# Optimization experiments

Measured on AMD Instinct MI355X. Metric: run time of the kernel, lower is better.

Reference implementation:

```python
import jax, jax.numpy as jnp
import numpy as np

ALPHA = 0.154
NUM_CLASSES = 50257
N = 4096

def setup_inputs() -> dict:
    key = jax.random.key(0)
    k1, k2 = jax.random.split(key)
    inputs = jax.random.normal(k1, (N, NUM_CLASSES), dtype=jnp.float32)
    targets = jax.random.randint(k2, (N,), 0, NUM_CLASSES, dtype=jnp.int64 if jax.config.jax_enable_x64 else jnp.int32)
    return {"inputs": inputs, "targets": targets}

def reference(inputs, targets):
    # softmax over classes (last dim), then probability at target class per row
    # log(softmax) computed stably via log_softmax (same math as log(softmax(x)))
    logp = jax.nn.log_softmax(inputs, axis=-1)           # [N, V]
    n = inputs.shape[0]
    logp_t = logp[jnp.arange(n), targets]                # [N], fused gather instead of NxN diag
    scale = 1.0 - ALPHA + ALPHA / float(inputs.shape[-1])
    out = logp_t + jnp.log(jnp.float32(scale))           # log(p_t * scale)
    return -jnp.mean(out)
```

## Files before the change

### kernel.cpp

```cpp
#include <hip/hip_runtime.h>
#include <cstdint>
#include <cstddef>

#define V 50257
#define BLOCK 256
#define UNROLL 8

__device__ __forceinline__ void combine(float& m, float& s, float mo, float so) {
    float m2 = fmaxf(m, mo);
    s = s * __expf(m - m2) + so * __expf(mo - m2);
    m = m2;
}

__device__ __forceinline__ float max4(const float4 v) {
    return fmaxf(fmaxf(v.x, v.y), fmaxf(v.z, v.w));
}

__device__ __forceinline__ float esum4(const float4 v, const float m2) {
    return (__expf(v.x - m2) + __expf(v.y - m2)) + (__expf(v.z - m2) + __expf(v.w - m2));
}

__global__ __launch_bounds__(BLOCK) void sce_row_kernel(
    const float* __restrict__ inputs, const int* __restrict__ targets,
    float* __restrict__ row_out) {
    const int row = blockIdx.x;
    const int tid = threadIdx.x;
    const float* row_ptr = inputs + (size_t)row * V;

    float xt = 0.0f;
    if (tid == 0) xt = row_ptr[targets[row]];

    const int misalign = (int)(((size_t)row * V) & 3);
    const int head = (4 - misalign) & 3;
    const int nvec = (V - head) >> 2;
    const int tail_start = head + (nvec << 2);
    const float4* vp = reinterpret_cast<const float4*>(row_ptr + head);

    float m = -INFINITY, s = 0.0f;

    int i = tid;
    for (; i + (UNROLL - 1) * BLOCK < nvec; i += UNROLL * BLOCK) {
        const float4 a0 = vp[i];
        const float4 a1 = vp[i + 1 * BLOCK];
        const float4 a2 = vp[i + 2 * BLOCK];
        const float4 a3 = vp[i + 3 * BLOCK];
        const float4 a4 = vp[i + 4 * BLOCK];
        const float4 a5 = vp[i + 5 * BLOCK];
        const float4 a6 = vp[i + 6 * BLOCK];
        const float4 a7 = vp[i + 7 * BLOCK];

        const float cm = fmaxf(
            fmaxf(fmaxf(max4(a0), max4(a1)), fmaxf(max4(a2), max4(a3))),
            fmaxf(fmaxf(max4(a4), max4(a5)), fmaxf(max4(a6), max4(a7))));
        const float m2 = fmaxf(m, cm);
        const float r = __expf(m - m2);
        const float e =
            ((esum4(a0, m2) + esum4(a1, m2)) + (esum4(a2, m2) + esum4(a3, m2))) +
            ((esum4(a4, m2) + esum4(a5, m2)) + (esum4(a6, m2) + esum4(a7, m2)));
        s = fmaf(s, r, e);
        m = m2;
    }
    for (; i < nvec; i += BLOCK) {
        const float4 v = vp[i];
        const float mv = max4(v);
        const float m2 = fmaxf(m, mv);
        s = fmaf(s, __expf(m - m2), esum4(v, m2));
        m = m2;
    }
    for (int j = tid; j < head; j += BLOCK) {
        const float v = row_ptr[j];
        const float m2 = fmaxf(m, v);
        s = s * __expf(m - m2) + __expf(v - m2);
        m = m2;
    }
    for (int j = tail_start + tid; j < V; j += BLOCK) {
        const float v = row_ptr[j];
        const float m2 = fmaxf(m, v);
        s = s * __expf(m - m2) + __expf(v - m2);
        m = m2;
    }

    for (int off = 32; off > 0; off >>= 1) {
        const float mo = __shfl_xor(m, off, 64);
        const float so = __shfl_xor(s, off, 64);
        combine(m, s, mo, so);
    }
    __shared__ float sm[BLOCK / 64], ss[BLOCK / 64];
    const int wave = tid >> 6;
    const int lane = tid & 63;
    if (lane == 0) { sm[wave] = m; ss[wave] = s; }
    __syncthreads();
    if (tid == 0) {
        m = sm[0]; s = ss[0];
        #pragma unroll
        for (int w = 1; w < BLOCK / 64; ++w) combine(m, s, sm[w], ss[w]);
        const float log_scale = logf((float)(1.0 - 0.154 + 0.154 / (double)V));
        row_out[row] = (xt - m - logf(s)) + log_scale;
    }
}

__global__ __launch_bounds__(BLOCK) void sce_final_kernel(
    const float* __restrict__ row_vals, float* __restrict__ out, int n) {
    float sum = 0.0f;
    for (int i = threadIdx.x; i < n; i += BLOCK) sum += row_vals[i];
    for (int off = 32; off > 0; off >>= 1) sum += __shfl_xor(sum, off, 64);
    __shared__ float ssum[BLOCK / 64];
    const int wave = threadIdx.x >> 6;
    const int lane = threadIdx.x & 63;
    if (lane == 0) ssum[wave] = sum;
    __syncthreads();
    if (threadIdx.x == 0) {
        float t = 0.0f;
        #pragma unroll
        for (int w = 0; w < BLOCK / 64; ++w) t += ssum[w];
        out[0] = -t / (float)n;
    }
}

extern "C" void kernel_launch(void* const* d_in, const int* in_sizes, int n_in,
                              void* d_out, int out_size, void* d_ws, size_t ws_size,
                              hipStream_t stream) {
    const float* inputs = (const float*)d_in[0];
    const int* targets = (const int*)d_in[1];
    float* out = (float*)d_out;
    const int n = in_sizes[1];
    float* row_vals = (float*)d_ws;

    sce_row_kernel<<<n, BLOCK, 0, stream>>>(inputs, targets, row_vals);
    sce_final_kernel<<<1, BLOCK, 0, stream>>>(row_vals, out, n);
}
```

Measured before the change: 1.024 ms.

## Split each row across two blocks and use nontemporal vector loads

Each row is now handled by two blocks, each computing a partial max and sum-exp over half the classes. The final kernel merges the two partials per row and adds the target logit. The aim is to double the number of blocks so the GPU holds more memory requests in flight and the per-block tail shrinks. Main loads also become nontemporal vector loads to avoid polluting the cache on a single streaming pass. The cost is extra workspace traffic and a slightly heavier final merge.

```diff
diff --git a/kernel.cpp b/kernel.cpp
--- a/kernel.cpp
+++ b/kernel.cpp
@@ -3,8 +3,11 @@
 #include <cstddef>
 
 #define V 50257
+#define HALF0 25128
 #define BLOCK 256
 #define UNROLL 8
+
+typedef float f32x4 __attribute__((ext_vector_type(4)));
 
 __device__ __forceinline__ void combine(float& m, float& s, float mo, float so) {
     float m2 = fmaxf(m, mo);
@@ -12,42 +15,48 @@
     m = m2;
 }
 
-__device__ __forceinline__ float max4(const float4 v) {
+__device__ __forceinline__ float max4(const f32x4 v) {
     return fmaxf(fmaxf(v.x, v.y), fmaxf(v.z, v.w));
 }
 
-__device__ __forceinline__ float esum4(const float4 v, const float m2) {
+__device__ __forceinline__ float esum4(const f32x4 v, const float m2) {
     return (__expf(v.x - m2) + __expf(v.y - m2)) + (__expf(v.z - m2) + __expf(v.w - m2));
 }
 
-__global__ __launch_bounds__(BLOCK) void sce_row_kernel(
+__global__ __launch_bounds__(BLOCK) void sce_partial_kernel(
     const float* __restrict__ inputs, const int* __restrict__ targets,
-    float* __restrict__ row_out) {
-    const int row = blockIdx.x;
+    float* __restrict__ pm, float* __restrict__ ps, float* __restrict__ pxt) {
+    const int bid = blockIdx.x;
+    const int row = bid >> 1;
+    const int half = bid & 1;
     const int tid = threadIdx.x;
     const float* row_ptr = inputs + (size_t)row * V;
 
-    float xt = 0.0f;
-    if (tid == 0) xt = row_ptr[targets[row]];
+    const int lo = half ? HALF0 : 0;
+    const int hi = half ? V : HALF0;
+    const float* ptr = row_ptr + lo;
+    const int len = hi - lo;
 
-    const int misalign = (int)(((size_t)row * V) & 3);
+    if (half == 0 && tid == 0) pxt[row] = row_ptr[targets[row]];
+
+    const int misalign = (int)(((size_t)row * V + (size_t)lo) & 3);
     const int head = (4 - misalign) & 3;
-    const int nvec = (V - head) >> 2;
+    const int nvec = (len - head) >> 2;
     const int tail_start = head + (nvec << 2);
-    const float4* vp = reinterpret_cast<const float4*>(row_ptr + head);
+    const f32x4* vp = reinterpret_cast<const f32x4*>(ptr + head);
 
     float m = -INFINITY, s = 0.0f;
 
     int i = tid;
     for (; i + (UNROLL - 1) * BLOCK < nvec; i += UNROLL * BLOCK) {
-        const float4 a0 = vp[i];
-        const float4 a1 = vp[i + 1 * BLOCK];
-        const float4 a2 = vp[i + 2 * BLOCK];
-        const float4 a3 = vp[i + 3 * BLOCK];
-        const float4 a4 = vp[i + 4 * BLOCK];
-        const float4 a5 = vp[i + 5 * BLOCK];
-        const float4 a6 = vp[i + 6 * BLOCK];
-        const float4 a7 = vp[i + 7 * BLOCK];
+        const f32x4 a0 = __builtin_nontemporal_load(vp + i);
+        const f32x4 a1 = __builtin_nontemporal_load(vp + i + 1 * BLOCK);
+        const f32x4 a2 = __builtin_nontemporal_load(vp + i + 2 * BLOCK);
+        const f32x4 a3 = __builtin_nontemporal_load(vp + i + 3 * BLOCK);
+        const f32x4 a4 = __builtin_nontemporal_load(vp + i + 4 * BLOCK);
+        const f32x4 a5 = __builtin_nontemporal_load(vp + i + 5 * BLOCK);
+        const f32x4 a6 = __builtin_nontemporal_load(vp + i + 6 * BLOCK);
+        const f32x4 a7 = __builtin_nontemporal_load(vp + i + 7 * BLOCK);
 
         const float cm = fmaxf(
             fmaxf(fmaxf(max4(a0), max4(a1)), fmaxf(max4(a2), max4(a3))),
@@ -61,20 +70,19 @@
         m = m2;
     }
     for (; i < nvec; i += BLOCK) {
-        const float4 v = vp[i];
-        const float mv = max4(v);
-        const float m2 = fmaxf(m, mv);
+        const f32x4 v = __builtin_nontemporal_load(vp + i);
+        const float m2 = fmaxf(m, max4(v));
         s = fmaf(s, __expf(m - m2), esum4(v, m2));
         m = m2;
     }
     for (int j = tid; j < head; j += BLOCK) {
-        const float v = row_ptr[j];
+        const float v = ptr[j];
         const float m2 = fmaxf(m, v);
         s = s * __expf(m - m2) + __expf(v - m2);
         m = m2;
     }
-    for (int j = tail_start + tid; j < V; j += BLOCK) {
-        const float v = row_ptr[j];
+    for (int j = tail_start + tid; j < len; j += BLOCK) {
+        const float v = ptr[j];
         const float m2 = fmaxf(m, v);
         s = s * __expf(m - m2) + __expf(v - m2);
         m = m2;
@@ -94,15 +102,23 @@
         m = sm[0]; s = ss[0];
         #pragma unroll
         for (int w = 1; w < BLOCK / 64; ++w) combine(m, s, sm[w], ss[w]);
-        const float log_scale = logf((float)(1.0 - 0.154 + 0.154 / (double)V));
-        row_out[row] = (xt - m - logf(s)) + log_scale;
+        pm[bid] = m;
+        ps[bid] = s;
     }
 }
 
 __global__ __launch_bounds__(BLOCK) void sce_final_kernel(
-    const float* __restrict__ row_vals, float* __restrict__ out, int n) {
+    const float* __restrict__ pm, const float* __restrict__ ps,
+    const float* __restrict__ pxt, float* __restrict__ out, int n) {
+    const float log_scale = logf((float)(1.0 - 0.154 + 0.154 / (double)V));
     float sum = 0.0f;
-    for (int i = threadIdx.x; i < n; i += BLOCK) sum += row_vals[i];
+    for (int r = threadIdx.x; r < n; r += BLOCK) {
+        const float m0 = pm[2 * r],     s0 = ps[2 * r];
+        const float m1 = pm[2 * r + 1], s1 = ps[2 * r + 1];
+        const float mm = fmaxf(m0, m1);
+        const float ssv = s0 * __expf(m0 - mm) + s1 * __expf(m1 - mm);
+        sum += (pxt[r] - mm - logf(ssv)) + log_scale;
+    }
     for (int off = 32; off > 0; off >>= 1) sum += __shfl_xor(sum, off, 64);
     __shared__ float ssum[BLOCK / 64];
     const int wave = threadIdx.x >> 6;
@@ -124,8 +140,11 @@
     const int* targets = (const int*)d_in[1];
     float* out = (float*)d_out;
     const int n = in_sizes[1];
-    float* row_vals = (float*)d_ws;
 
-    sce_row_kernel<<<n, BLOCK, 0, stream>>>(inputs, targets, row_vals);
-    sce_final_kernel<<<1, BLOCK, 0, stream>>>(row_vals, out, n);
+    float* pm  = (float*)d_ws;
+    float* ps  = pm + 2 * n;
+    float* pxt = ps + 2 * n;
+
+    sce_partial_kernel<<<2 * n, BLOCK, 0, stream>>>(inputs, targets, pm, ps, pxt);
+    sce_final_kernel<<<1, BLOCK, 0, stream>>>(pm, ps, pxt, out, n);
 }
```

After: 991.3 us. 1.03x faster.
